# Kernel tuning notes

Measured on AMD Instinct MI355X. Metric: run time of the kernel, lower is better.

The kernel has to match this reference:

```python
import jax, jax.numpy as jnp
import numpy as np

NUM_CLUSTERS = 64  # real clusters (ghost clusters excluded from residuals)
EPS = 1e-12        # F.normalize eps


def setup_inputs() -> dict:
    key = jax.random.key(0)
    k1, k2, k3 = jax.random.split(key, 3)
    x = jax.random.normal(k1, (8, 128, 32, 32), dtype=jnp.float32)
    # 1x1 conv weight [K+G, C] (kernel spatial dims squeezed), no bias (vladv2=False)
    conv_w = jax.random.normal(k2, (68, 128), dtype=jnp.float32) * 0.05
    centroids = jax.random.uniform(k3, (68, 128), dtype=jnp.float32)
    return {"x": x, "conv_w": conv_w, "centroids": centroids}


def reference(x, conv_w, centroids):
    # x: [N,C,H,W]; conv_w: [K+G,C]; centroids: [K+G,C]
    # descriptor-wise L2 normalization over channel dim (normalize_input=True)
    nrm = jnp.sqrt(jnp.sum(x * x, axis=1, keepdims=True))
    xn = x / jnp.maximum(nrm, EPS)
    # 1x1 conv -> soft assignment logits over K+G clusters, softmax over cluster dim
    logits = jnp.einsum('nchw,kc->nkhw', xn, conv_w)
    soft_assign = jax.nn.softmax(logits, axis=1)            # [N,K+G,H,W]
    # fused per-cluster residual: (x - c_k) * a_k, only real clusters
    resid = (xn[:, None, :, :, :] -
             centroids[:NUM_CLUSTERS][None, :, :, None, None])  # [N,K,C,H,W]
    store_residual = resid * soft_assign[:, :NUM_CLUSTERS, None, :, :]
    return store_residual, soft_assign
```

## Files before the change

kernel.cpp:

```cpp
#include <hip/hip_runtime.h>

#define PIMG 1024
#define CCH  128
#define KG   68
#define KR   64
#define T1   32
#define WP   132
#define LP   33

typedef float f4v __attribute__((ext_vector_type(4)));

__global__ __launch_bounds__(512) void nv_assign_kernel(
    const float* __restrict__ x,
    const float* __restrict__ conv_w,
    float* __restrict__ sa_out,
    float* __restrict__ rnorm_ws)
{
    __shared__ float xs[CCH * T1];
    __shared__ float wl[KG * WP];
    __shared__ float lg[KG * LP];
    __shared__ float red[16 * T1];
    __shared__ float rn_l[T1];
    __shared__ float mx_l[T1];
    __shared__ float is_l[T1];

    const int t   = threadIdx.x;
    const int gp0 = blockIdx.x * T1;
    const int n   = gp0 >> 10;
    const int p0  = gp0 & 1023;

    for (int i = t; i < KG * (CCH / 4); i += 512) {
        int k = i >> 5, c4 = i & 31;
        *(f4v*)(wl + k * WP + c4 * 4) = ((const f4v*)(conv_w + k * CCH))[c4];
    }
    const float* xb = x + (size_t)n * (CCH * PIMG) + p0;
    for (int i = t; i < CCH * (T1 / 4); i += 512) {
        int c = i >> 3, p4 = i & 7;
        *(f4v*)(xs + c * T1 + p4 * 4) = *(const f4v*)(xb + c * PIMG + p4 * 4);
    }
    __syncthreads();

    {
        int pix = t & 31, q = t >> 5;
        float s = 0.f;
        #pragma unroll
        for (int c = q * 8; c < q * 8 + 8; ++c) {
            float v = xs[c * T1 + pix];
            s += v * v;
        }
        red[q * T1 + pix] = s;
    }
    __syncthreads();
    if (t < T1) {
        float s = 0.f;
        #pragma unroll
        for (int q = 0; q < 16; ++q) s += red[q * T1 + t];
        float r = 1.0f / fmaxf(sqrtf(s), 1e-12f);
        rn_l[t] = r;
        rnorm_ws[gp0 + t] = r;
    }
    __syncthreads();

    for (int task = t; task < KG * 8; task += 512) {
        int g = task & 7, k = task >> 3;
        const float* wr = wl + k * WP;
        const float* xr = xs + g * 4;
        f4v acc = {0.f, 0.f, 0.f, 0.f};
        #pragma unroll 8
        for (int c0 = 0; c0 < CCH; c0 += 4) {
            f4v w4 = *(const f4v*)(wr + c0);
            acc += *(const f4v*)(xr + (c0 + 0) * T1) * w4.x;
            acc += *(const f4v*)(xr + (c0 + 1) * T1) * w4.y;
            acc += *(const f4v*)(xr + (c0 + 2) * T1) * w4.z;
            acc += *(const f4v*)(xr + (c0 + 3) * T1) * w4.w;
        }
        f4v r4 = *(const f4v*)(rn_l + g * 4);
        acc *= r4;
        float* lr = lg + k * LP + g * 4;
        lr[0] = acc.x; lr[1] = acc.y; lr[2] = acc.z; lr[3] = acc.w;
    }
    __syncthreads();

    {
        int pix = t & 31, q = t >> 5;
        float m = -1e30f;
        for (int k = q; k < KG; k += 16) m = fmaxf(m, lg[k * LP + pix]);
        red[q * T1 + pix] = m;
    }
    __syncthreads();
    if (t < T1) {
        float m = red[t];
        #pragma unroll
        for (int q = 1; q < 16; ++q) m = fmaxf(m, red[q * T1 + t]);
        mx_l[t] = m;
    }
    __syncthreads();
    {
        int pix = t & 31, q = t >> 5;
        float m = mx_l[pix], s = 0.f;
        for (int k = q; k < KG; k += 16) {
            float e = expf(lg[k * LP + pix] - m);
            lg[k * LP + pix] = e;
            s += e;
        }
        red[q * T1 + pix] = s;
    }
    __syncthreads();
    if (t < T1) {
        float s = 0.f;
        #pragma unroll
        for (int q = 0; q < 16; ++q) s += red[q * T1 + t];
        is_l[t] = 1.0f / s;
    }
    __syncthreads();

    for (int i = t; i < KG * T1; i += 512) {
        int k = i >> 5, pix = i & 31;
        sa_out[((size_t)n * KG + k) * PIMG + p0 + pix] = lg[k * LP + pix] * is_l[pix];
    }
}

__global__ __launch_bounds__(256) void nv_resid_kernel(
    const float* __restrict__ x,
    const float* __restrict__ centroids,
    const float* __restrict__ sa,
    const float* __restrict__ rnorm,
    float* __restrict__ out)
{
    const int b  = blockIdx.x;
    const int n  = b >> 8;
    const int k  = (b >> 2) & 63;
    const int c0 = (b & 3) << 5;
    const int t  = threadIdx.x;

    const f4v rn4 = ((const f4v*)(rnorm + (size_t)n * PIMG))[t];
    const f4v a4  = ((const f4v*)(sa + ((size_t)n * KG + k) * PIMG))[t];
    const f4v ra  = rn4 * a4;

    const float* cw = centroids + k * CCH + c0;
    const float* xb = x + (size_t)n * (CCH * PIMG) + (size_t)c0 * PIMG;
    float* ob = out + (((size_t)n * KR + k) * CCH + c0) * PIMG;

    #pragma unroll 8
    for (int c = 0; c < 32; ++c) {
        f4v xv = ((const f4v*)(xb + c * PIMG))[t];
        float ce = cw[c];
        f4v o = xv * ra - ce * a4;
        ((f4v*)(ob + c * PIMG))[t] = o;
    }
}

extern "C" void kernel_launch(void* const* d_in, const int* in_sizes, int n_in,
                              void* d_out, int out_size, void* d_ws, size_t ws_size,
                              hipStream_t stream) {
    const float* x         = (const float*)d_in[0];
    const float* conv_w    = (const float*)d_in[1];
    const float* centroids = (const float*)d_in[2];

    const int N = in_sizes[0] / (CCH * PIMG);

    float* out    = (float*)d_out;
    float* sa_out = out + (size_t)N * KR * CCH * PIMG;
    float* rnorm  = (float*)d_ws;

    nv_assign_kernel<<<N * (PIMG / T1), 512, 0, stream>>>(x, conv_w, sa_out, rnorm);
    nv_resid_kernel<<<N * KR * 4, 256, 0, stream>>>(x, centroids, sa_out, rnorm, out);
}
```

Baseline: 62.13 us.

## Fuse soft-assignment and residual kernels into one kernel writing from shared memory

Merges the assignment kernel and the residual kernel into a single kernel. Each block pre-normalizes its 32-pixel x tile in shared memory, computes the softmax, keeps it in shared memory, and writes all 64x128 residual rows for its pixels directly. This removes the second launch, the re-read of x and soft-assign from global memory, and the rnorm workspace. In exchange, each residual write covers only 128 contiguous bytes per row instead of full 4KB rows. The grid also shrinks to 256 large blocks, which may reduce write efficiency and occupancy on a store-bound workload.

```diff
diff --git a/kernel.cpp b/kernel.cpp
--- a/kernel.cpp
+++ b/kernel.cpp
@@ -5,18 +5,20 @@
 #define KG   68
 #define KR   64
 #define T1   32
+#define XP   36
 #define WP   132
-#define LP   33
+#define LP   36
 
 typedef float f4v __attribute__((ext_vector_type(4)));
 
-__global__ __launch_bounds__(512) void nv_assign_kernel(
+__global__ __launch_bounds__(512) void nv_fused_kernel(
     const float* __restrict__ x,
     const float* __restrict__ conv_w,
-    float* __restrict__ sa_out,
-    float* __restrict__ rnorm_ws)
+    const float* __restrict__ centroids,
+    float* __restrict__ out,
+    float* __restrict__ sa_out)
 {
-    __shared__ float xs[CCH * T1];
+    __shared__ float xs[CCH * XP];
     __shared__ float wl[KG * WP];
     __shared__ float lg[KG * LP];
     __shared__ float red[16 * T1];
@@ -34,9 +36,9 @@
         *(f4v*)(wl + k * WP + c4 * 4) = ((const f4v*)(conv_w + k * CCH))[c4];
     }
     const float* xb = x + (size_t)n * (CCH * PIMG) + p0;
-    for (int i = t; i < CCH * (T1 / 4); i += 512) {
-        int c = i >> 3, p4 = i & 7;
-        *(f4v*)(xs + c * T1 + p4 * 4) = *(const f4v*)(xb + c * PIMG + p4 * 4);
+    for (int i = t; i < CCH * T1; i += 512) {
+        int c = i >> 5, pix = i & 31;
+        xs[c * XP + pix] = xb[c * PIMG + pix];
     }
     __syncthreads();
 
@@ -45,7 +47,7 @@
         float s = 0.f;
         #pragma unroll
         for (int c = q * 8; c < q * 8 + 8; ++c) {
-            float v = xs[c * T1 + pix];
+            float v = xs[c * XP + pix];
             s += v * v;
         }
         red[q * T1 + pix] = s;
@@ -55,9 +57,12 @@
         float s = 0.f;
         #pragma unroll
         for (int q = 0; q < 16; ++q) s += red[q * T1 + t];
-        float r = 1.0f / fmaxf(sqrtf(s), 1e-12f);
-        rn_l[t] = r;
-        rnorm_ws[gp0 + t] = r;
+        rn_l[t] = 1.0f / fmaxf(sqrtf(s), 1e-12f);
+    }
+    __syncthreads();
+    for (int i = t; i < CCH * T1; i += 512) {
+        int pix = i & 31;
+        xs[(i >> 5) * XP + pix] *= rn_l[pix];
     }
     __syncthreads();
 
@@ -69,13 +74,11 @@
         #pragma unroll 8
         for (int c0 = 0; c0 < CCH; c0 += 4) {
             f4v w4 = *(const f4v*)(wr + c0);
-            acc += *(const f4v*)(xr + (c0 + 0) * T1) * w4.x;
-            acc += *(const f4v*)(xr + (c0 + 1) * T1) * w4.y;
-            acc += *(const f4v*)(xr + (c0 + 2) * T1) * w4.z;
-            acc += *(const f4v*)(xr + (c0 + 3) * T1) * w4.w;
+            acc += *(const f4v*)(xr + (c0 + 0) * XP) * w4.x;
+            acc += *(const f4v*)(xr + (c0 + 1) * XP) * w4.y;
+            acc += *(const f4v*)(xr + (c0 + 2) * XP) * w4.z;
+            acc += *(const f4v*)(xr + (c0 + 3) * XP) * w4.w;
         }
-        f4v r4 = *(const f4v*)(rn_l + g * 4);
-        acc *= r4;
         float* lr = lg + k * LP + g * 4;
         lr[0] = acc.x; lr[1] = acc.y; lr[2] = acc.z; lr[3] = acc.w;
     }
@@ -116,37 +119,25 @@
 
     for (int i = t; i < KG * T1; i += 512) {
         int k = i >> 5, pix = i & 31;
-        sa_out[((size_t)n * KG + k) * PIMG + p0 + pix] = lg[k * LP + pix] * is_l[pix];
+        float v = lg[k * LP + pix] * is_l[pix];
+        lg[k * LP + pix] = v;
+        sa_out[((size_t)n * KG + k) * PIMG + p0 + pix] = v;
     }
-}
+    __syncthreads();
 
-__global__ __launch_bounds__(256) void nv_resid_kernel(
-    const float* __restrict__ x,
-    const float* __restrict__ centroids,
-    const float* __restrict__ sa,
-    const float* __restrict__ rnorm,
-    float* __restrict__ out)
-{
-    const int b  = blockIdx.x;
-    const int n  = b >> 8;
-    const int k  = (b >> 2) & 63;
-    const int c0 = (b & 3) << 5;
-    const int t  = threadIdx.x;
-
-    const f4v rn4 = ((const f4v*)(rnorm + (size_t)n * PIMG))[t];
-    const f4v a4  = ((const f4v*)(sa + ((size_t)n * KG + k) * PIMG))[t];
-    const f4v ra  = rn4 * a4;
-
-    const float* cw = centroids + k * CCH + c0;
-    const float* xb = x + (size_t)n * (CCH * PIMG) + (size_t)c0 * PIMG;
-    float* ob = out + (((size_t)n * KR + k) * CCH + c0) * PIMG;
-
-    #pragma unroll 8
-    for (int c = 0; c < 32; ++c) {
-        f4v xv = ((const f4v*)(xb + c * PIMG))[t];
-        float ce = cw[c];
-        f4v o = xv * ra - ce * a4;
-        ((f4v*)(ob + c * PIMG))[t] = o;
+    {
+        const int g = t & 7, kc0 = t >> 3;
+        float* ob = out + (size_t)n * (KR * CCH * PIMG) + p0 + g * 4;
+        #pragma unroll 4
+        for (int r = 0; r < 128; ++r) {
+            int kc = r * 64 + kc0;
+            int k = kc >> 7, c = kc & 127;
+            float ce = centroids[k * CCH + c];
+            f4v xn4 = *(const f4v*)(xs + c * XP + g * 4);
+            f4v a4  = *(const f4v*)(lg + k * LP + g * 4);
+            f4v o = (xn4 - ce) * a4;
+            *(f4v*)(ob + (size_t)kc * PIMG) = o;
+        }
     }
 }
 
@@ -161,8 +152,7 @@
 
     float* out    = (float*)d_out;
     float* sa_out = out + (size_t)N * KR * CCH * PIMG;
-    float* rnorm  = (float*)d_ws;
 
-    nv_assign_kernel<<<N * (PIMG / T1), 512, 0, stream>>>(x, conv_w, sa_out, rnorm);
-    nv_resid_kernel<<<N * KR * 4, 256, 0, stream>>>(x, centroids, sa_out, rnorm, out);
+    nv_fused_kernel<<<N * (PIMG / T1), 512, 0, stream>>>(
+        x, conv_w, centroids, out, sa_out);
 }
```

Measured after the change: 57.22 us. 7.9% less time.
